# Kernel tuning notes

Measured on AMD Instinct MI355X. Metric: run time of the kernel, lower is better.

## Reference

```python
import jax, jax.numpy as jnp
import numpy as np

N = 8192
DIM_A = 512
DIM_B = 512
HID = 64
MOTIVE = 64


def setup_inputs() -> dict:
    key = jax.random.key(0)
    ks = jax.random.split(key, 10)
    s = lambda fan_in: 1.0 / np.sqrt(fan_in)
    return {
        "X_A": jax.random.normal(ks[0], (N, DIM_A), jnp.float32),
        "X_B": jax.random.normal(ks[1], (N, DIM_B), jnp.float32),
        "WA1": jax.random.uniform(ks[2], (DIM_A, HID), jnp.float32, -s(DIM_A), s(DIM_A)),
        "bA1": jnp.zeros((HID,), jnp.float32),
        "WA2": jax.random.uniform(ks[3], (HID, MOTIVE), jnp.float32, -s(HID), s(HID)),
        "bA2": jnp.zeros((MOTIVE,), jnp.float32),
        "WB1": jax.random.uniform(ks[4], (DIM_B, HID), jnp.float32, -s(DIM_B), s(DIM_B)),
        "bB1": jnp.zeros((HID,), jnp.float32),
        "WB2": jax.random.uniform(ks[5], (HID, MOTIVE), jnp.float32, -s(HID), s(HID)),
        "bB2": jnp.zeros((MOTIVE,), jnp.float32),
    }


def _functor(x, W1, b1, W2, b2):
    return jax.nn.relu(x @ W1 + b1) @ W2 + b2


def _sq_cdist(x, y):
    # squared euclidean distance matrix [N, N]; clamp for numerical safety
    xx = jnp.sum(x * x, axis=-1)[:, None]
    yy = jnp.sum(y * y, axis=-1)[None, :]
    return jnp.maximum(xx + yy - 2.0 * (x @ y.T), 0.0)


def reference(X_A, X_B, WA1, bA1, WA2, bA2, WB1, bB1, WB2, bB2):
    M_A = _functor(X_A, WA1, bA1, WA2, bA2)  # [N, motive_dim]
    M_B = _functor(X_B, WB1, bB1, WB2, bB2)
    sigma = 1.0
    inv = 1.0 / (2.0 * sigma ** 2)
    k_xx = jnp.exp(-_sq_cdist(M_A, M_A) * inv).mean()
    k_yy = jnp.exp(-_sq_cdist(M_B, M_B) * inv).mean()
    k_xy = jnp.exp(-_sq_cdist(M_A, M_B) * inv).mean()
    mmd_loss = k_xx + k_yy - 2.0 * k_xy
    return (mmd_loss, M_A, M_B)
```

## Files before the change

### kernel.cpp

```cpp
#include <hip/hip_runtime.h>
#include <hip/hip_bf16.h>
#include <cstdint>
#include <cstddef>

#define N_ROWS 8192
#define DIM_IN 512
#define MOT 64
#define INV_N2 (1.0f / (8192.0f * 8192.0f))
#define PAIR_GRID 512

typedef __attribute__((ext_vector_type(8))) short bf16x8;
typedef __attribute__((ext_vector_type(4))) float f32x4;

__device__ inline unsigned short f2bf(float f) {
    union { __hip_bfloat16 h; unsigned short u; } cv;
    cv.h = __float2bfloat16(f);
    return cv.u;
}
__device__ inline float bfbits2f(unsigned short u) {
    union { unsigned int i; float f; } cv;
    cv.i = ((unsigned int)u) << 16;
    return cv.f;
}
__device__ inline void gl_lds16(const void* g, void* l) {
    __builtin_amdgcn_global_load_lds(
        (const __attribute__((address_space(1))) unsigned int*)g,
        (__attribute__((address_space(3))) unsigned int*)l, 16, 0, 0);
}
__device__ inline void gl_lds4(const void* g, void* l) {
    __builtin_amdgcn_global_load_lds(
        (const __attribute__((address_space(1))) unsigned int*)g,
        (__attribute__((address_space(3))) unsigned int*)l, 4, 0, 0);
}

__global__ __launch_bounds__(256) void functor2_kernel(
    const float* __restrict__ XA, const float* __restrict__ WA1, const float* __restrict__ bA1,
    const float* __restrict__ WA2, const float* __restrict__ bA2,
    const float* __restrict__ XB, const float* __restrict__ WB1, const float* __restrict__ bB1,
    const float* __restrict__ WB2, const float* __restrict__ bB2,
    float* __restrict__ MA, float* __restrict__ MB,
    float* __restrict__ nAo, float* __restrict__ nBo,
    unsigned short* __restrict__ PbfA, unsigned short* __restrict__ PbfB)
{
    const int half = blockIdx.x >> 8;
    const float* X  = half ? XB  : XA;
    const float* W1 = half ? WB1 : WA1;
    const float* b1 = half ? bB1 : bA1;
    const float* W2 = half ? WB2 : WA2;
    const float* b2 = half ? bB2 : bA2;
    float* Mout  = half ? MB  : MA;
    float* norms = half ? nBo : nAo;
    unsigned short* Pbf = half ? PbfB : PbfA;

    __shared__ float XsT[64][34];
    __shared__ float Ws[64][64];
    __shared__ float HsT[64][34];

    const int t  = threadIdx.x;
    const int tx = t & 15;
    const int ty = t >> 4;
    const int row0 = (blockIdx.x & 255) * 32;

    float c[2][4] = {};

    for (int kc = 0; kc < DIM_IN; kc += 64) {
        #pragma unroll
        for (int q = 0; q < 2; ++q) {
            int idx = q * 256 + t;
            int row = idx >> 4;
            int k4  = (idx & 15) << 2;
            float4 v = *(const float4*)&X[(size_t)(row0 + row) * DIM_IN + kc + k4];
            XsT[k4 + 0][row] = v.x;
            XsT[k4 + 1][row] = v.y;
            XsT[k4 + 2][row] = v.z;
            XsT[k4 + 3][row] = v.w;
        }
        #pragma unroll
        for (int q = 0; q < 4; ++q) {
            int idx = q * 256 + t;
            int row = idx >> 4;
            int k4  = (idx & 15) << 2;
            *(float4*)&Ws[row][k4] = *(const float4*)&W1[(size_t)(kc + row) * MOT + k4];
        }
        __syncthreads();
        #pragma unroll 8
        for (int k = 0; k < 64; ++k) {
            float2 a = *(const float2*)&XsT[k][ty * 2];
            float4 b = *(const float4*)&Ws[k][tx * 4];
            float av[2] = {a.x, a.y};
            float bv[4] = {b.x, b.y, b.z, b.w};
            #pragma unroll
            for (int i = 0; i < 2; ++i)
                #pragma unroll
                for (int j = 0; j < 4; ++j)
                    c[i][j] = fmaf(av[i], bv[j], c[i][j]);
        }
        __syncthreads();
    }

    {
        float bias1[4];
        #pragma unroll
        for (int j = 0; j < 4; ++j) bias1[j] = b1[tx * 4 + j];
        #pragma unroll
        for (int i = 0; i < 2; ++i)
            #pragma unroll
            for (int j = 0; j < 4; ++j) {
                float h = c[i][j] + bias1[j];
                HsT[tx * 4 + j][ty * 2 + i] = fmaxf(h, 0.0f);
                c[i][j] = 0.0f;
            }
    }

    #pragma unroll
    for (int q = 0; q < 4; ++q) {
        int idx = q * 256 + t;
        int row = idx >> 4;
        int k4  = (idx & 15) << 2;
        *(float4*)&Ws[row][k4] = *(const float4*)&W2[(size_t)row * MOT + k4];
    }
    __syncthreads();

    #pragma unroll 8
    for (int k = 0; k < 64; ++k) {
        float2 a = *(const float2*)&HsT[k][ty * 2];
        float4 b = *(const float4*)&Ws[k][tx * 4];
        float av[2] = {a.x, a.y};
        float bv[4] = {b.x, b.y, b.z, b.w};
        #pragma unroll
        for (int i = 0; i < 2; ++i)
            #pragma unroll
            for (int j = 0; j < 4; ++j)
                c[i][j] = fmaf(av[i], bv[j], c[i][j]);
    }

    float bias2[4];
    #pragma unroll
    for (int j = 0; j < 4; ++j) bias2[j] = b2[tx * 4 + j];

    float p[2] = {0.0f, 0.0f};
    #pragma unroll
    for (int i = 0; i < 2; ++i) {
        unsigned short q4[4];
        int grow = row0 + ty * 2 + i;
        #pragma unroll
        for (int j = 0; j < 4; ++j) {
            float m = c[i][j] + bias2[j];
            Mout[(size_t)grow * MOT + tx * 4 + j] = m;
            q4[j] = f2bf(m);
            float mn = bfbits2f(q4[j]);
            p[i] = fmaf(mn, mn, p[i]);
        }
        int r = grow & 127;
        size_t tile = (size_t)(grow >> 7);
        int swz = (tx * 8) ^ ((r & 7) << 4);
        ushort4 v; v.x = q4[0]; v.y = q4[1]; v.z = q4[2]; v.w = q4[3];
        *(ushort4*)((char*)Pbf + tile * 16384 + (size_t)r * 128 + swz) = v;
    }
    #pragma unroll
    for (int off = 1; off < 16; off <<= 1)
        #pragma unroll
        for (int i = 0; i < 2; ++i)
            p[i] += __shfl_xor(p[i], off, 64);
    if (tx == 0) {
        norms[row0 + ty * 2 + 0] = p[0];
        norms[row0 + ty * 2 + 1] = p[1];
    }
}

__device__ inline void decode_tile(int id, int T, int TRI, int& which, int& bi, int& bj) {
    if (id < 2 * TRI) {
        which = (id < TRI) ? 0 : 1;
        if (which) id -= TRI;
        int r = (int)((sqrtf(8.0f * (float)id + 1.0f) - 1.0f) * 0.5f);
        while ((r + 1) * (r + 2) / 2 <= id) ++r;
        while (r * (r + 1) / 2 > id) --r;
        bi = r;
        bj = id - r * (r + 1) / 2;
    } else {
        id -= 2 * TRI;
        which = 2;
        bi = id >> 6;
        bj = id & (T - 1);
    }
}

__global__ __launch_bounds__(256) void pair_persist_kernel(
    const unsigned short* __restrict__ PA, const unsigned short* __restrict__ PB,
    const float* __restrict__ nA, const float* __restrict__ nB,
    float* __restrict__ out0)
{
    const int T   = N_ROWS / 128;
    const int TRI = T * (T + 1) / 2;
    const int NT  = 2 * TRI + T * T;

    __shared__ unsigned short As[2][8192];
    __shared__ unsigned short Bs[2][8192];
    __shared__ float nAsh[2][128];
    __shared__ float nBsh[2][128];
    __shared__ float red[4];

    const int t    = threadIdx.x;
    const int lane = t & 63;
    const int wave = t >> 6;
    const int wr   = wave >> 1, wc = wave & 1;

    auto stage = [&](int nb, int swhich, int sbi, int sbj) {
        const unsigned short* P = (swhich == 1) ? PB : PA;
        const unsigned short* Q = (swhich == 0) ? PA : PB;
        const char* srcA = (const char*)P + (size_t)sbi * 16384 + wave * 1024 + lane * 16;
        const char* srcB = (const char*)Q + (size_t)sbj * 16384 + wave * 1024 + lane * 16;
        char* ldsA = (char*)&As[nb][0] + wave * 1024;
        char* ldsB = (char*)&Bs[nb][0] + wave * 1024;
        #pragma unroll
        for (int p4 = 0; p4 < 4; ++p4) {
            gl_lds16(srcA + p4 * 4096, ldsA + p4 * 4096);
            gl_lds16(srcB + p4 * 4096, ldsB + p4 * 4096);
        }
        const float* nP = (swhich == 1) ? nB : nA;
        const float* nQ = (swhich == 0) ? nA : nB;
        if (wave == 0) {
            gl_lds4(&nP[sbi * 128 + lane], &nAsh[nb][0]);
            gl_lds4(&nP[sbi * 128 + 64 + lane], &nAsh[nb][64]);
        }
        if (wave == 1) {
            gl_lds4(&nQ[sbj * 128 + lane], &nBsh[nb][0]);
            gl_lds4(&nQ[sbj * 128 + 64 + lane], &nBsh[nb][64]);
        }
    };

    int tid = blockIdx.x;
    int which, bi, bj;
    decode_tile(tid, T, TRI, which, bi, bj);
    stage(0, which, bi, bj);

    const int sw = (lane & 7) << 4;
    const int kb = (lane >> 4) << 4;

    float s_acc = 0.0f;
    int it = 0;
    while (true) {
        const int cur = it & 1;
        const int cwhich = which, cbi = bi, cbj = bj;

        __syncthreads();

        const int ntid = tid + PAIR_GRID;
        if (ntid < NT) {
            decode_tile(ntid, T, TRI, which, bi, bj);
            stage(cur ^ 1, which, bi, bj);
        }

        const char* Ab = (const char*)&As[cur][0];
        const char* Bb = (const char*)&Bs[cur][0];
        f32x4 acc[4][4] = {};
        #pragma unroll
        for (int k0 = 0; k0 < 2; ++k0) {
            const int koff = (k0 * 64 + kb) ^ sw;
            bf16x8 af[4], bf[4];
            #pragma unroll
            for (int i = 0; i < 4; ++i)
                af[i] = *(const bf16x8*)(Ab + (wr * 64 + i * 16 + (lane & 15)) * 128 + koff);
            #pragma unroll
            for (int j = 0; j < 4; ++j)
                bf[j] = *(const bf16x8*)(Bb + (wc * 64 + j * 16 + (lane & 15)) * 128 + koff);
            #pragma unroll
            for (int i = 0; i < 4; ++i)
                #pragma unroll
                for (int j = 0; j < 4; ++j)
                    acc[i][j] = __builtin_amdgcn_mfma_f32_16x16x32_bf16(af[i], bf[j], acc[i][j], 0, 0, 0);
        }

        float cAn[4][4], cBn[4];
        #pragma unroll
        for (int i = 0; i < 4; ++i) {
            float4 n4 = *(const float4*)&nAsh[cur][wr * 64 + i * 16 + ((lane >> 4) << 2)];
            cAn[i][0] = 0.5f * n4.x; cAn[i][1] = 0.5f * n4.y;
            cAn[i][2] = 0.5f * n4.z; cAn[i][3] = 0.5f * n4.w;
        }
        #pragma unroll
        for (int j = 0; j < 4; ++j)
            cBn[j] = 0.5f * nBsh[cur][wc * 64 + j * 16 + (lane & 15)];

        float stile = 0.0f;
        if (cwhich != 2 && cbi == cbj) {
            #pragma unroll
            for (int i = 0; i < 4; ++i)
                #pragma unroll
                for (int j = 0; j < 4; ++j)
                    #pragma unroll
                    for (int r = 0; r < 4; ++r) {
                        float tv = acc[i][j][r] - cAn[i][r] - cBn[j];
                        stile += __expf(fminf(tv, 0.0f));
                    }
        } else {
            #pragma unroll
            for (int i = 0; i < 4; ++i)
                #pragma unroll
                for (int j = 0; j < 4; ++j)
                    #pragma unroll
                    for (int r = 0; r < 4; ++r) {
                        float tv = acc[i][j][r] - cAn[i][r] - cBn[j];
                        stile += __expf(tv);
                    }
        }

        float scale = (cwhich == 2) ? (-2.0f * INV_N2)
                                    : ((cbi != cbj) ? (2.0f * INV_N2) : INV_N2);
        s_acc = fmaf(scale, stile, s_acc);

        if (ntid >= NT) break;
        tid = ntid; ++it;
    }

    #pragma unroll
    for (int off = 32; off > 0; off >>= 1) s_acc += __shfl_xor(s_acc, off, 64);
    if (lane == 0) red[wave] = s_acc;
    __syncthreads();
    if (t == 0) atomicAdd(out0, red[0] + red[1] + red[2] + red[3]);
}

extern "C" void kernel_launch(void* const* d_in, const int* in_sizes, int n_in,
                              void* d_out, int out_size, void* d_ws, size_t ws_size,
                              hipStream_t stream)
{
    const float* XA  = (const float*)d_in[0];
    const float* XB  = (const float*)d_in[1];
    const float* WA1 = (const float*)d_in[2];
    const float* bA1 = (const float*)d_in[3];
    const float* WA2 = (const float*)d_in[4];
    const float* bA2 = (const float*)d_in[5];
    const float* WB1 = (const float*)d_in[6];
    const float* bB1 = (const float*)d_in[7];
    const float* WB2 = (const float*)d_in[8];
    const float* bB2 = (const float*)d_in[9];

    float* out = (float*)d_out;
    float* MA  = out + 1;
    float* MB  = out + 1 + (size_t)N_ROWS * MOT;
    float* nA  = (float*)d_ws;
    float* nB  = nA + N_ROWS;
    unsigned short* PA = (unsigned short*)(nB + N_ROWS);
    unsigned short* PB = PA + (size_t)N_ROWS * MOT;

    hipMemsetAsync(d_out, 0, sizeof(float), stream);

    functor2_kernel<<<512, 256, 0, stream>>>(XA, WA1, bA1, WA2, bA2,
                                             XB, WB1, bB1, WB2, bB2,
                                             MA, MB, nA, nB, PA, PB);

    pair_persist_kernel<<<PAIR_GRID, 256, 0, stream>>>(PA, PB, nA, nB, out);
}
```

Baseline: 78.89 us.

## Assign contiguous tile chunks per block and keep A fragments in registers

Replaces the strided persistent tile schedule with contiguous chunks of 16 tiles per block, so the row-block A operand stays in registers and is reloaded from global only when the row changes. Only the B tile and its norms are double-buffered through LDS, which halves LDS staging. The exp is rewritten as exp2 with log2(e) folded into an fma, and split accumulators are used. The risk is that the A reloads at row boundaries are synchronous global loads that are not overlapped.

```diff
diff --git a/kernel.cpp b/kernel.cpp
--- a/kernel.cpp
+++ b/kernel.cpp
@@ -7,7 +7,8 @@
 #define DIM_IN 512
 #define MOT 64
 #define INV_N2 (1.0f / (8192.0f * 8192.0f))
-#define PAIR_GRID 512
+#define CHUNK 16
+#define PAIR_BLOCKS 516
 
 typedef __attribute__((ext_vector_type(8))) short bf16x8;
 typedef __attribute__((ext_vector_type(4))) float f32x4;
@@ -185,18 +186,25 @@
     }
 }
 
-__global__ __launch_bounds__(256) void pair_persist_kernel(
+__device__ inline void step_tile(int& which, int& bi, int& bj, int T) {
+    ++bj;
+    if (which == 2) {
+        if (bj == T) { bj = 0; ++bi; }
+    } else {
+        if (bj > bi) { bj = 0; ++bi; if (bi == T) { bi = 0; ++which; } }
+    }
+}
+
+__global__ __launch_bounds__(256, 3) void pair_persist2_kernel(
     const unsigned short* __restrict__ PA, const unsigned short* __restrict__ PB,
     const float* __restrict__ nA, const float* __restrict__ nB,
     float* __restrict__ out0)
 {
     const int T   = N_ROWS / 128;
     const int TRI = T * (T + 1) / 2;
-    const int NT  = 2 * TRI + T * T;
-
-    __shared__ unsigned short As[2][8192];
+    const float L2E = 1.44269504088896341f;
+
     __shared__ unsigned short Bs[2][8192];
-    __shared__ float nAsh[2][128];
     __shared__ float nBsh[2][128];
     __shared__ float red[4];
 
@@ -204,94 +212,93 @@
     const int lane = t & 63;
     const int wave = t >> 6;
     const int wr   = wave >> 1, wc = wave & 1;
-
-    auto stage = [&](int nb, int swhich, int sbi, int sbj) {
-        const unsigned short* P = (swhich == 1) ? PB : PA;
-        const unsigned short* Q = (swhich == 0) ? PA : PB;
-        const char* srcA = (const char*)P + (size_t)sbi * 16384 + wave * 1024 + lane * 16;
-        const char* srcB = (const char*)Q + (size_t)sbj * 16384 + wave * 1024 + lane * 16;
-        char* ldsA = (char*)&As[nb][0] + wave * 1024;
-        char* ldsB = (char*)&Bs[nb][0] + wave * 1024;
-        #pragma unroll
-        for (int p4 = 0; p4 < 4; ++p4) {
-            gl_lds16(srcA + p4 * 4096, ldsA + p4 * 4096);
-            gl_lds16(srcB + p4 * 4096, ldsB + p4 * 4096);
-        }
-        const float* nP = (swhich == 1) ? nB : nA;
-        const float* nQ = (swhich == 0) ? nA : nB;
+    const int sw   = (lane & 7) << 4;
+    const int kb   = (lane >> 4) << 4;
+
+    bf16x8 af[4][2];
+    float  negA[4][4];
+
+    auto loadA = [&](int w_, int bi_) {
+        const unsigned short* P = (w_ == 1) ? PB : PA;
+        const float* nP         = (w_ == 1) ? nB : nA;
+        const char* base = (const char*)P + (size_t)bi_ * 16384;
+        #pragma unroll
+        for (int i = 0; i < 4; ++i) {
+            const char* rowp = base + (size_t)(wr * 64 + i * 16 + (lane & 15)) * 128;
+            #pragma unroll
+            for (int k0 = 0; k0 < 2; ++k0)
+                af[i][k0] = *(const bf16x8*)(rowp + ((k0 * 64 + kb) ^ sw));
+            float4 n4 = *(const float4*)&nP[bi_ * 128 + wr * 64 + i * 16 + ((lane >> 4) << 2)];
+            negA[i][0] = -0.5f * L2E * n4.x;
+            negA[i][1] = -0.5f * L2E * n4.y;
+            negA[i][2] = -0.5f * L2E * n4.z;
+            negA[i][3] = -0.5f * L2E * n4.w;
+        }
+    };
+
+    auto stageB = [&](int nb, int w_, int bj_) {
+        const unsigned short* Q = (w_ == 0) ? PA : PB;
+        const float* nQ         = (w_ == 0) ? nA : nB;
+        const char* src = (const char*)Q + (size_t)bj_ * 16384 + wave * 1024 + lane * 16;
+        char* dst = (char*)&Bs[nb][0] + wave * 1024;
+        #pragma unroll
+        for (int p4 = 0; p4 < 4; ++p4)
+            gl_lds16(src + p4 * 4096, dst + p4 * 4096);
         if (wave == 0) {
-            gl_lds4(&nP[sbi * 128 + lane], &nAsh[nb][0]);
-            gl_lds4(&nP[sbi * 128 + 64 + lane], &nAsh[nb][64]);
-        }
-        if (wave == 1) {
-            gl_lds4(&nQ[sbj * 128 + lane], &nBsh[nb][0]);
-            gl_lds4(&nQ[sbj * 128 + 64 + lane], &nBsh[nb][64]);
+            gl_lds4(&nQ[bj_ * 128 + lane],      &nBsh[nb][0]);
+            gl_lds4(&nQ[bj_ * 128 + 64 + lane], &nBsh[nb][64]);
         }
     };
 
-    int tid = blockIdx.x;
-    int which, bi, bj;
-    decode_tile(tid, T, TRI, which, bi, bj);
-    stage(0, which, bi, bj);
-
-    const int sw = (lane & 7) << 4;
-    const int kb = (lane >> 4) << 4;
+    int cw, cbi, cbj;
+    decode_tile(blockIdx.x * CHUNK, T, TRI, cw, cbi, cbj);
+    loadA(cw, cbi);
+    stageB(0, cw, cbj);
 
     float s_acc = 0.0f;
-    int it = 0;
-    while (true) {
-        const int cur = it & 1;
-        const int cwhich = which, cbi = bi, cbj = bj;
-
+
+    for (int u = 0; u < CHUNK; ++u) {
+        const int cur = u & 1;
         __syncthreads();
 
-        const int ntid = tid + PAIR_GRID;
-        if (ntid < NT) {
-            decode_tile(ntid, T, TRI, which, bi, bj);
-            stage(cur ^ 1, which, bi, bj);
-        }
-
-        const char* Ab = (const char*)&As[cur][0];
+        int nw = cw, nbi = cbi, nbj = cbj;
+        const bool havenext = (u + 1 < CHUNK);
+        if (havenext) {
+            step_tile(nw, nbi, nbj, T);
+            stageB(cur ^ 1, nw, nbj);
+        }
+
         const char* Bb = (const char*)&Bs[cur][0];
         f32x4 acc[4][4] = {};
         #pragma unroll
         for (int k0 = 0; k0 < 2; ++k0) {
             const int koff = (k0 * 64 + kb) ^ sw;
-            bf16x8 af[4], bf[4];
-            #pragma unroll
-            for (int i = 0; i < 4; ++i)
-                af[i] = *(const bf16x8*)(Ab + (wr * 64 + i * 16 + (lane & 15)) * 128 + koff);
+            bf16x8 bfr[4];
             #pragma unroll
             for (int j = 0; j < 4; ++j)
-                bf[j] = *(const bf16x8*)(Bb + (wc * 64 + j * 16 + (lane & 15)) * 128 + koff);
+                bfr[j] = *(const bf16x8*)(Bb + (wc * 64 + j * 16 + (lane & 15)) * 128 + koff);
             #pragma unroll
             for (int i = 0; i < 4; ++i)
                 #pragma unroll
                 for (int j = 0; j < 4; ++j)
-                    acc[i][j] = __builtin_amdgcn_mfma_f32_16x16x32_bf16(af[i], bf[j], acc[i][j], 0, 0, 0);
-        }
-
-        float cAn[4][4], cBn[4];
-        #pragma unroll
-        for (int i = 0; i < 4; ++i) {
-            float4 n4 = *(const float4*)&nAsh[cur][wr * 64 + i * 16 + ((lane >> 4) << 2)];
-            cAn[i][0] = 0.5f * n4.x; cAn[i][1] = 0.5f * n4.y;
-            cAn[i][2] = 0.5f * n4.z; cAn[i][3] = 0.5f * n4.w;
-        }
+                    acc[i][j] = __builtin_amdgcn_mfma_f32_16x16x32_bf16(af[i][k0], bfr[j], acc[i][j], 0, 0, 0);
+        }
+
+        float posB[4];
         #pragma unroll
         for (int j = 0; j < 4; ++j)
-            cBn[j] = 0.5f * nBsh[cur][wc * 64 + j * 16 + (lane & 15)];
-
-        float stile = 0.0f;
-        if (cwhich != 2 && cbi == cbj) {
+            posB[j] = 0.5f * L2E * nBsh[cur][wc * 64 + j * 16 + (lane & 15)];
+
+        float sa[4] = {0.0f, 0.0f, 0.0f, 0.0f};
+        if (cw != 2 && cbi == cbj) {
             #pragma unroll
             for (int i = 0; i < 4; ++i)
                 #pragma unroll
                 for (int j = 0; j < 4; ++j)
                     #pragma unroll
                     for (int r = 0; r < 4; ++r) {
-                        float tv = acc[i][j][r] - cAn[i][r] - cBn[j];
-                        stile += __expf(fminf(tv, 0.0f));
+                        float tv = fmaf(acc[i][j][r], L2E, negA[i][r]) - posB[j];
+                        sa[j] += exp2f(fminf(tv, 0.0f));
                     }
         } else {
             #pragma unroll
@@ -300,17 +307,20 @@
                 for (int j = 0; j < 4; ++j)
                     #pragma unroll
                     for (int r = 0; r < 4; ++r) {
-                        float tv = acc[i][j][r] - cAn[i][r] - cBn[j];
-                        stile += __expf(tv);
+                        float tv = fmaf(acc[i][j][r], L2E, negA[i][r]) - posB[j];
+                        sa[j] += exp2f(tv);
                     }
         }
-
-        float scale = (cwhich == 2) ? (-2.0f * INV_N2)
-                                    : ((cbi != cbj) ? (2.0f * INV_N2) : INV_N2);
+        float stile = (sa[0] + sa[1]) + (sa[2] + sa[3]);
+
+        float scale = (cw == 2) ? (-2.0f * INV_N2)
+                                : ((cbi != cbj) ? (2.0f * INV_N2) : INV_N2);
         s_acc = fmaf(scale, stile, s_acc);
 
-        if (ntid >= NT) break;
-        tid = ntid; ++it;
+        if (havenext) {
+            if (nw != cw || nbi != cbi) loadA(nw, nbi);
+            cw = nw; cbi = nbi; cbj = nbj;
+        }
     }
 
     #pragma unroll
@@ -349,5 +359,5 @@
                                              XB, WB1, bB1, WB2, bB2,
                                              MA, MB, nA, nB, PA, PB);
 
-    pair_persist_kernel<<<PAIR_GRID, 256, 0, stream>>>(PA, PB, nA, nB, out);
-}
+    pair_persist2_kernel<<<PAIR_BLOCKS, 256, 0, stream>>>(PA, PB, nA, nB, out);
+}
```

After: 110.9 us. 40.6% more time.
